# Kernel tuning notes

Measured on AMD Instinct MI355X. Metric: run time of the kernel, lower is better.

The kernel has to match this reference:

```python
import jax, jax.numpy as jnp
import numpy as np

DIM, HEADS, DHEAD = 256, 8, 64
INNER = HEADS * DHEAD
EPS = 1e-5


def _ln(x, g, b):
    m = x.mean(-1, keepdims=True)
    v = ((x - m) ** 2).mean(-1, keepdims=True)
    return (x - m) / jnp.sqrt(v + EPS) * g + b


def setup_inputs() -> dict:
    key = jax.random.key(0)
    ks = jax.random.split(key, 24)
    b, n, Q, K = 1, 6, 900, 1408
    d = DIM
    s = lambda fan_in: 1.0 / np.sqrt(fan_in)
    inp = {
        "k_g": jax.random.normal(ks[0], (b, n, K, d), jnp.float32),
        "q_g": jax.random.normal(ks[1], (b, n, Q, d), jnp.float32),
        "k_a": jax.random.normal(ks[2], (b, n, K, d), jnp.float32),
        "q_a": jax.random.normal(ks[3], (b, Q, d), jnp.float32),
        "v": jax.random.normal(ks[4], (b, n, K, d), jnp.float32),
        "mask": jax.random.randint(ks[5], (b, n, K), 0, 2).astype(bool),
        # projections (stored as (in, out))
        "W_qg": jax.random.uniform(ks[6], (d, INNER), jnp.float32, -s(d), s(d)),
        "b_qg": jnp.zeros((INNER,), jnp.float32),
        "W_kg": jax.random.uniform(ks[7], (d, INNER), jnp.float32, -s(d), s(d)),
        "b_kg": jnp.zeros((INNER,), jnp.float32),
        "W_qa": jax.random.uniform(ks[8], (d, INNER), jnp.float32, -s(d), s(d)),
        "b_qa": jnp.zeros((INNER,), jnp.float32),
        "W_ka": jax.random.uniform(ks[9], (d, INNER), jnp.float32, -s(d), s(d)),
        "b_ka": jnp.zeros((INNER,), jnp.float32),
        "W_v": jax.random.uniform(ks[10], (d, INNER), jnp.float32, -s(d), s(d)),
        "b_v": jnp.zeros((INNER,), jnp.float32),
        "W_o": jax.random.uniform(ks[11], (INNER, d), jnp.float32, -s(INNER), s(INNER)),
        "b_o": jnp.zeros((d,), jnp.float32),
        "ln1_g": jnp.ones((d,), jnp.float32),
        "ln1_b": jnp.zeros((d,), jnp.float32),
        "W_m1": jax.random.uniform(ks[12], (d, 2 * d), jnp.float32, -s(d), s(d)),
        "b_m1": jnp.zeros((2 * d,), jnp.float32),
        "W_m2": jax.random.uniform(ks[13], (2 * d, d), jnp.float32, -s(2 * d), s(2 * d)),
        "b_m2": jnp.zeros((d,), jnp.float32),
        "ln2_g": jnp.ones((d,), jnp.float32),
        "ln2_b": jnp.zeros((d,), jnp.float32),
        "scale_g": jnp.full((HEADS,), DHEAD ** -0.5, jnp.float32),
        "scale_a": jnp.full((HEADS,), DHEAD ** -0.5, jnp.float32),
    }
    return inp


def reference(k_g, q_g, k_a, q_a, v, mask,
              W_qg, b_qg, W_kg, b_kg, W_qa, b_qa, W_ka, b_ka, W_v, b_v,
              W_o, b_o, ln1_g, ln1_b, W_m1, b_m1, W_m2, b_m2, ln2_g, ln2_b,
              scale_g, scale_a):
    b, n, Q, _ = q_g.shape
    K = k_g.shape[2]
    h, dh = HEADS, DHEAD
    skip = q_a

    def split(x):  # (..., h*dh) -> (b, h, ..., dh)
        return jnp.moveaxis(x.reshape(x.shape[:-1] + (h, dh)), -2, 1)

    kg = split(k_g @ W_kg + b_kg)          # (b, h, n, K, dh)
    qg = split(q_g @ W_qg + b_qg)          # (b, h, n, Q, dh)
    ka = split(k_a @ W_ka + b_ka)          # (b, h, n, K, dh)
    qa = split(q_a @ W_qa + b_qa)          # (b, h, Q, dh)
    vv = split(v @ W_v + b_v)              # (b, h, n, K, dh)

    dot_g = jnp.einsum('bhnqd,bhnkd->bhnqk', qg, kg)
    dot_a = jnp.einsum('bhqd,bhnkd->bhnqk', qa, ka)
    sg = scale_g[None, :, None, None, None]
    sa = scale_a[None, :, None, None, None]
    dot = sg * dot_g + sa * dot_a
    dot = jnp.where(mask[:, None, :, None, :], -jnp.inf, dot)

    # softmax jointly over (n, K)
    dot = dot.transpose(0, 1, 3, 2, 4).reshape(b, h, Q, n * K)
    att = jax.nn.softmax(dot, axis=-1)
    vflat = vv.reshape(b, h, n * K, dh)
    a = jnp.einsum('bhqk,bhkd->bhqd', att, vflat)
    a = a.transpose(0, 2, 1, 3).reshape(b, Q, h * dh)

    z = a @ W_o + b_o + skip
    z = _ln(z, ln1_g, ln1_b)
    z = z + (jax.nn.gelu(z @ W_m1 + b_m1, approximate=False) @ W_m2 + b_m2)
    z = _ln(z, ln2_g, ln2_b)
    return z
```

## Files before the change

kernel.cpp:

```cpp
#include <hip/hip_runtime.h>
#include <stdint.h>

typedef unsigned short u16;
typedef _Float16 half8 __attribute__((ext_vector_type(8)));
typedef float f32x4 __attribute__((ext_vector_type(4)));

__device__ __forceinline__ u16 f2h(float f) {
    _Float16 h = (_Float16)f; u16 u; __builtin_memcpy(&u, &h, 2); return u;
}
__device__ __forceinline__ float h2f(u16 u) {
    _Float16 h; __builtin_memcpy(&h, &u, 2); return (float)h;
}

template<int CTRL>
__device__ __forceinline__ float dppf(float x) {
    return __builtin_bit_cast(float,
        __builtin_amdgcn_update_dpp(0, __builtin_bit_cast(int, x), CTRL, 0xF, 0xF, false));
}
__device__ __forceinline__ float sum16(float x) {
    x += dppf<0xB1>(x);
    x += dppf<0x4E>(x);
    x += dppf<0x124>(x);
    x += dppf<0x128>(x);
    return x;
}

__global__ __launch_bounds__(256) void prep_kernel(
    const float* __restrict__ W_qg, const float* __restrict__ W_kg,
    const float* __restrict__ W_qa, const float* __restrict__ W_ka,
    const float* __restrict__ W_v,  const float* __restrict__ W_o,
    const float* __restrict__ W_m1, const float* __restrict__ W_m2,
    u16* __restrict__ T_qg, u16* __restrict__ T_kg, u16* __restrict__ T_qa,
    u16* __restrict__ T_ka, u16* __restrict__ T_v,  u16* __restrict__ T_o,
    u16* __restrict__ T_m1, u16* __restrict__ T_m2,
    const float* __restrict__ scale_g, const float* __restrict__ scale_a,
    const float* __restrict__ b_kg, const float* __restrict__ b_ka,
    float* __restrict__ bkg_s, float* __restrict__ bka_s,
    const int* __restrict__ mask, int* __restrict__ mflag)
{
    const int z = blockIdx.z;
    const int tid = threadIdx.x;
    if (z == 8) {
        if (blockIdx.y != 0) return;
        if (blockIdx.x == 0) {
            __shared__ int f;
            if (tid == 0) f = 0;
            __syncthreads();
            int local = 0;
            for (int i = tid; i < 2112; i += 256) { int vv = mask[i]; if (vv & ~1) local = 1; }
            if (local) atomicOr(&f, 1);
            __syncthreads();
            if (tid == 0) *mflag = f;
        } else if (blockIdx.x == 1) {
            for (int j = tid; j < 512; j += 256) {
                bkg_s[j] = b_kg[j] * scale_g[j >> 6];
                bka_s[j] = b_ka[j] * scale_a[j >> 6];
            }
        }
        return;
    }
    const int K = (z == 5 || z == 7) ? 512 : 256;
    const int N = (z == 5 || z == 7) ? 256 : 512;
    const int k0 = blockIdx.x * 64, n0 = blockIdx.y * 64;
    if (k0 >= K || n0 >= N) return;
    const float* W = z==0?W_qg: z==1?W_kg: z==2?W_qa: z==3?W_ka: z==4?W_v: z==5?W_o: z==6?W_m1: W_m2;
    u16* D        = z==0?T_qg: z==1?T_kg: z==2?T_qa: z==3?T_ka: z==4?T_v: z==5?T_o: z==6?T_m1: T_m2;
    const float* scp = z==1 ? scale_g : z==3 ? scale_a : nullptr;

    __shared__ u16 T[64][80];
    const int cr = tid >> 4, cc = (tid & 15) * 4;
    const float sc = scp ? scp[(n0 + cc) >> 6] : 1.0f;
    #pragma unroll
    for (int i = 0; i < 4; ++i) {
        const int r = cr + i * 16;
        const float4 vv = *(const float4*)(W + (size_t)(k0 + r) * N + n0 + cc);
        T[cc + 0][r] = f2h(vv.x * sc);
        T[cc + 1][r] = f2h(vv.y * sc);
        T[cc + 2][r] = f2h(vv.z * sc);
        T[cc + 3][r] = f2h(vv.w * sc);
    }
    __syncthreads();
    const int nr = tid >> 2, part = (tid & 3) * 16;
    u16* drow = D + (size_t)(n0 + nr) * K + k0 + part;
    *(half8*)(drow)     = *(const half8*)&T[nr][part];
    *(half8*)(drow + 8) = *(const half8*)&T[nr][part + 8];
}

__global__ __launch_bounds__(256, 4) void proj_all(
    const float* __restrict__ k_g, const float* __restrict__ k_a,
    const float* __restrict__ v,   const float* __restrict__ q_g,
    const float* __restrict__ q_a,
    const u16* __restrict__ T_kg, const u16* __restrict__ T_ka,
    const u16* __restrict__ T_v,  const u16* __restrict__ T_qg,
    const u16* __restrict__ T_qa,
    const float* __restrict__ bkg_s, const float* __restrict__ bka_s,
    const float* __restrict__ b_v,   const float* __restrict__ b_qg,
    const float* __restrict__ b_qa,
    u16* __restrict__ qcat, u16* __restrict__ kcat, u16* __restrict__ vt)
{
    __shared__ u16 Ws[256 * 36];

    int bx = blockIdx.x;
    int mode, M;
    const float* X; const u16* Wt; const float* bias; u16* out;
    if (bx < 132)      { mode = 2; M = 8448; X = k_g; Wt = T_kg; bias = bkg_s; out = kcat; }
    else if (bx < 264) { mode = 3; M = 8448; X = k_a; Wt = T_ka; bias = bka_s; out = kcat; bx -= 132; }
    else if (bx < 396) { mode = 4; M = 8448; X = v;   Wt = T_v;  bias = b_v;   out = vt;   bx -= 264; }
    else if (bx < 481) { mode = 0; M = 5400; X = q_g; Wt = T_qg; bias = b_qg;  out = qcat; bx -= 396; }
    else               { mode = 1; M = 900;  X = q_a; Wt = T_qa; bias = b_qa;  out = qcat; bx -= 481; }
    const int rows_per_n = (mode == 0) ? 900 : 1408;

    const int tid = threadIdx.x;
    const int w = tid >> 6, lane = tid & 63;
    const int l15 = lane & 15, quad = lane >> 4;
    const int m0 = bx * 64;
    const int nbase = blockIdx.y * 256;
    const int row = m0 + w * 16 + l15;

    const float* xrow = X + (size_t)(row < M ? row : 0) * 256 + quad * 8;
    const u16* wcol = Wt + ((size_t)(nbase + tid) << 8);

    f32x4 o[4][4];
    #pragma unroll
    for (int nt = 0; nt < 4; ++nt)
        #pragma unroll
        for (int t = 0; t < 4; ++t) { o[nt][t][0]=0.f; o[nt][t][1]=0.f; o[nt][t][2]=0.f; o[nt][t][3]=0.f; }

    for (int k0 = 0; k0 < 8; ++k0) {
        {
            const uint4 w0 = *(const uint4*)(wcol + k0 * 32 + 0);
            const uint4 w1 = *(const uint4*)(wcol + k0 * 32 + 8);
            const uint4 w2 = *(const uint4*)(wcol + k0 * 32 + 16);
            const uint4 w3 = *(const uint4*)(wcol + k0 * 32 + 24);
            *(uint4*)&Ws[tid * 36 + 0]  = w0;
            *(uint4*)&Ws[tid * 36 + 8]  = w1;
            *(uint4*)&Ws[tid * 36 + 16] = w2;
            *(uint4*)&Ws[tid * 36 + 24] = w3;
        }
        __syncthreads();

        const float4 a0 = *(const float4*)(xrow + k0 * 32);
        const float4 a1 = *(const float4*)(xrow + k0 * 32 + 4);
        half8 af;
        af[0]=(_Float16)a0.x; af[1]=(_Float16)a0.y; af[2]=(_Float16)a0.z; af[3]=(_Float16)a0.w;
        af[4]=(_Float16)a1.x; af[5]=(_Float16)a1.y; af[6]=(_Float16)a1.z; af[7]=(_Float16)a1.w;

        #pragma unroll
        for (int nt = 0; nt < 4; ++nt)
            #pragma unroll
            for (int t = 0; t < 4; ++t) {
                const half8 bf = *(const half8*)&Ws[(nt * 64 + t * 16 + l15) * 36 + quad * 8];
                o[nt][t] = __builtin_amdgcn_mfma_f32_16x16x32_f16(af, bf, o[nt][t], 0, 0, 0);
            }
        __syncthreads();
    }

    #pragma unroll
    for (int nt = 0; nt < 4; ++nt) {
        const int n0 = nbase + nt * 64;
        const int hh = n0 >> 6;
        float bj[4];
        #pragma unroll
        for (int t = 0; t < 4; ++t) bj[t] = bias[n0 + t * 16 + l15];

        if (mode == 4) {
            const int gr0 = m0 + w * 16 + quad * 4;
            if (gr0 < M) {
                const int nI = gr0 / rows_per_n;
                const int rr = gr0 - nI * rows_per_n;
                u16* vb = out + (size_t)(hh * 6 + nI) * 64 * 1408;
                #pragma unroll
                for (int t = 0; t < 4; ++t) {
                    const int d = t * 16 + l15;
                    ushort4 pk;
                    pk.x = f2h(o[nt][t][0] + bj[t]);
                    pk.y = f2h(o[nt][t][1] + bj[t]);
                    pk.z = f2h(o[nt][t][2] + bj[t]);
                    pk.w = f2h(o[nt][t][3] + bj[t]);
                    *(ushort4*)&vb[(size_t)d * 1408 + rr] = pk;
                }
            }
        } else if (mode == 1) {
            #pragma unroll
            for (int r = 0; r < 4; ++r) {
                const int gr = m0 + w * 16 + quad * 4 + r;
                if (gr < M) {
                    for (int nb = 0; nb < 6; ++nb) {
                        u16* qb = out + (((size_t)(hh * 6 + nb) * 900 + gr) << 7) + 64;
                        #pragma unroll
                        for (int t = 0; t < 4; ++t)
                            qb[t * 16 + l15] = f2h(o[nt][t][r] + bj[t]);
                    }
                }
            }
        } else {
            const size_t kdim = (mode == 0) ? 900 : 1408;
            const int doff = (mode == 3) ? 64 : 0;
            #pragma unroll
            for (int r = 0; r < 4; ++r) {
                const int gr = m0 + w * 16 + quad * 4 + r;
                if (gr < M) {
                    const int nI = gr / rows_per_n;
                    const int rr = gr - nI * rows_per_n;
                    u16* ob = out + (((size_t)(hh * 6 + nI) * kdim + rr) << 7) + doff;
                    #pragma unroll
                    for (int t = 0; t < 4; ++t)
                        ob[t * 16 + l15] = f2h(o[nt][t][r] + bj[t]);
                }
            }
        }
    }
}

__global__ __launch_bounds__(256, 4) void attn_kernel(
    const u16* __restrict__ qcat, const u16* __restrict__ kcat,
    const u16* __restrict__ vt, const void* __restrict__ maskp,
    const int* __restrict__ mflag,
    u16* __restrict__ Opart, float* __restrict__ lpart)
{
    __shared__ __align__(16) u16 Ks[64 * 136];
    __shared__ __align__(16) u16 Vs[64 * 72];
    __shared__ __align__(16) u16 Ps[4][1216];
    __shared__ float Mb[64];

    const int flat = blockIdx.x;
    const int grp = flat >> 3;
    const int qt = grp % 15;
    const int rest = grp / 15;
    const int hn_i = (flat & 7) + 8 * (rest % 6);
    const int sp = rest / 6;
    const int h = hn_i / 6, n = hn_i - h * 6;
    (void)h;

    const int q0 = qt * 64;
    const int tid = threadIdx.x;
    const int w = tid >> 6, lane = tid & 63;
    const int l15 = lane & 15, quad = lane >> 4;
    const bool m8 = (*mflag != 0);
    const size_t hn = (size_t)hn_i;

    const u16* kbase = kcat + ((hn * 1408) << 7);
    const u16* vbase = vt + hn * 64 * 1408;
    const unsigned char* mB = (const unsigned char*)maskp;
    const int* mI = (const int*)maskp;
    const int mko = n * 1408;

    const int krow_s = tid >> 4;
    const int kcol_s = (tid & 15) * 8;
    const int vrow_s = tid >> 3;
    const int vcol_s = (tid & 7) * 8;

    half8 qf[4];
    {
        const int gq = q0 + w * 16 + l15;
        if (gq < 900) {
            const u16* qrow = qcat + ((hn * 900 + gq) << 7) + quad * 8;
            #pragma unroll
            for (int k0 = 0; k0 < 4; ++k0)
                qf[k0] = *(const half8*)(qrow + k0 * 32);
        } else {
            #pragma unroll
            for (int k0 = 0; k0 < 4; ++k0)
                #pragma unroll
                for (int j = 0; j < 8; ++j) qf[k0][j] = (_Float16)0.0f;
        }
    }

    half8 onesb;
    {
        const _Float16 ov = (l15 == 0) ? (_Float16)1.0f : (_Float16)0.0f;
        #pragma unroll
        for (int j = 0; j < 8; ++j) onesb[j] = ov;
    }

    f32x4 o[4];
    f32x4 l16;
    #pragma unroll
    for (int t = 0; t < 4; ++t) { o[t][0]=0.f; o[t][1]=0.f; o[t][2]=0.f; o[t][3]=0.f; }
    l16[0]=0.f; l16[1]=0.f; l16[2]=0.f; l16[3]=0.f;

    uint4 kA, kB, kC, kD, vA, vB;
    float mreg = 0.0f;
    {
        const int k0c = (sp * 11) * 64;
        kA = *(const uint4*)(kbase + ((size_t)(k0c +  0 + krow_s) << 7) + kcol_s);
        kB = *(const uint4*)(kbase + ((size_t)(k0c + 16 + krow_s) << 7) + kcol_s);
        kC = *(const uint4*)(kbase + ((size_t)(k0c + 32 + krow_s) << 7) + kcol_s);
        kD = *(const uint4*)(kbase + ((size_t)(k0c + 48 + krow_s) << 7) + kcol_s);
        vA = *(const uint4*)(vbase + (size_t)(vrow_s)      * 1408 + k0c + vcol_s);
        vB = *(const uint4*)(vbase + (size_t)(32 + vrow_s) * 1408 + k0c + vcol_s);
        if (tid < 64) {
            const int ki = mko + k0c + tid;
            const int mv = m8 ? (int)mB[ki] : mI[ki];
            mreg = mv ? -1e30f : 0.0f;
        }
    }

    for (int cc = 0; cc < 11; ++cc) {
        *(uint4*)&Ks[( 0 + krow_s) * 136 + kcol_s] = kA;
        *(uint4*)&Ks[(16 + krow_s) * 136 + kcol_s] = kB;
        *(uint4*)&Ks[(32 + krow_s) * 136 + kcol_s] = kC;
        *(uint4*)&Ks[(48 + krow_s) * 136 + kcol_s] = kD;
        *(uint4*)&Vs[(vrow_s)      * 72 + vcol_s] = vA;
        *(uint4*)&Vs[(32 + vrow_s) * 72 + vcol_s] = vB;
        if (tid < 64) Mb[tid] = mreg;
        __syncthreads();

        if (cc < 10) {
            const int k0n = (sp * 11 + cc + 1) * 64;
            kA = *(const uint4*)(kbase + ((size_t)(k0n +  0 + krow_s) << 7) + kcol_s);
            kB = *(const uint4*)(kbase + ((size_t)(k0n + 16 + krow_s) << 7) + kcol_s);
            kC = *(const uint4*)(kbase + ((size_t)(k0n + 32 + krow_s) << 7) + kcol_s);
            kD = *(const uint4*)(kbase + ((size_t)(k0n + 48 + krow_s) << 7) + kcol_s);
            vA = *(const uint4*)(vbase + (size_t)(vrow_s)      * 1408 + k0n + vcol_s);
            vB = *(const uint4*)(vbase + (size_t)(32 + vrow_s) * 1408 + k0n + vcol_s);
            if (tid < 64) {
                const int ki = mko + k0n + tid;
                const int mv = m8 ? (int)mB[ki] : mI[ki];
                mreg = mv ? -1e30f : 0.0f;
            }
        }

        f32x4 s[4];
        #pragma unroll
        for (int t = 0; t < 4; ++t) {
            const float mbv = Mb[t * 16 + l15];
            s[t][0]=mbv; s[t][1]=mbv; s[t][2]=mbv; s[t][3]=mbv;
        }
        #pragma unroll
        for (int k0 = 0; k0 < 4; ++k0)
            #pragma unroll
            for (int t = 0; t < 4; ++t) {
                const half8 kf = *(const half8*)&Ks[(t * 16 + l15) * 136 + k0 * 32 + quad * 8];
                s[t] = __builtin_amdgcn_mfma_f32_16x16x32_f16(qf[k0], kf, s[t], 0, 0, 0);
            }

        #pragma unroll
        for (int r = 0; r < 4; ++r) {
            const float p0 = __expf(s[0][r]);
            const float p1 = __expf(s[1][r]);
            const float p2 = __expf(s[2][r]);
            const float p3 = __expf(s[3][r]);
            u16* pr = &Ps[w][(quad * 4 + r) * 72 + quad * 16 + l15];
            pr[0]  = f2h(p0);
            pr[16] = f2h(p1);
            pr[32] = f2h(p2);
            pr[48] = f2h(p3);
        }

        const u16* prow = &Ps[w][l15 * 72 + (l15 >> 2) * 16 + quad * 8];
        const half8 pa0 = *(const half8*)(prow);
        const half8 pa1 = *(const half8*)(prow + 32);

        l16 = __builtin_amdgcn_mfma_f32_16x16x32_f16(pa0, onesb, l16, 0, 0, 0);
        l16 = __builtin_amdgcn_mfma_f32_16x16x32_f16(pa1, onesb, l16, 0, 0, 0);

        #pragma unroll
        for (int t = 0; t < 4; ++t) {
            const half8 v0 = *(const half8*)&Vs[(t * 16 + l15) * 72 + quad * 8];
            const half8 v1 = *(const half8*)&Vs[(t * 16 + l15) * 72 + 32 + quad * 8];
            o[t] = __builtin_amdgcn_mfma_f32_16x16x32_f16(pa0, v0, o[t], 0, 0, 0);
            o[t] = __builtin_amdgcn_mfma_f32_16x16x32_f16(pa1, v1, o[t], 0, 0, 0);
        }
        __syncthreads();
    }

    const int p = sp * 48 + hn_i;
    #pragma unroll
    for (int r = 0; r < 4; ++r) {
        const int gq = q0 + w * 16 + quad * 4 + r;
        if (gq < 900) {
            u16* db = Opart + ((size_t)p * 900 + gq) * 64 + l15;
            db[0]  = f2h(o[0][r]);
            db[16] = f2h(o[1][r]);
            db[32] = f2h(o[2][r]);
            db[48] = f2h(o[3][r]);
            if (l15 == 0) lpart[p * 900 + gq] = l16[r];
        }
    }
}

__global__ __launch_bounds__(256) void combine_kernel(
    const u16* __restrict__ Opart, const float* __restrict__ lpart,
    u16* __restrict__ a16)
{
    const int g = blockIdx.x * 256 + threadIdx.x;
    const int h = g / 57600;
    const int r = g - h * 57600;
    const int q = r >> 6;
    const int d = r & 63;
    float l = 0.f, ov = 0.f;
    #pragma unroll
    for (int s = 0; s < 12; ++s) {
        const int p = (s >> 1) + h * 6 + ((s & 1) ? 48 : 0);
        l  += lpart[p * 900 + q];
        ov += h2f(Opart[((size_t)p * 900 + q) * 64 + d]);
    }
    a16[(size_t)q * 512 + h * 64 + d] = f2h(ov / fmaxf(l, 1e-30f));
}

__global__ __launch_bounds__(256) void epi_mega(
    const u16* __restrict__ a16, const u16* __restrict__ T_o,
    const u16* __restrict__ T_m1, const u16* __restrict__ T_m2,
    const float* __restrict__ b_o, const float* __restrict__ q_a,
    const float* __restrict__ ln1_g, const float* __restrict__ ln1_b,
    const float* __restrict__ b_m1, const float* __restrict__ b_m2,
    const float* __restrict__ ln2_g, const float* __restrict__ ln2_b,
    float* __restrict__ outf)
{
    __shared__ u16 Z1[16][264];
    __shared__ u16 H[16][520];
    __shared__ float Ssum[4][16];
    __shared__ float Ssq[4][16];

    const int tid = threadIdx.x;
    const int w = tid >> 6, lane = tid & 63;
    const int l15 = lane & 15, quad = lane >> 4;
    const int m0 = blockIdx.x * 16;

    {
        const int ar = m0 + l15;
        const u16* arow = a16 + (size_t)(ar < 900 ? ar : 899) * 512 + quad * 8;

        f32x4 acc[4];
        #pragma unroll
        for (int t = 0; t < 4; ++t) { acc[t][0]=0.f; acc[t][1]=0.f; acc[t][2]=0.f; acc[t][3]=0.f; }

        #pragma unroll
        for (int k0 = 0; k0 < 16; ++k0) {
            const half8 af = *(const half8*)(arow + k0 * 32);
            #pragma unroll
            for (int t = 0; t < 4; ++t) {
                const int nn = w * 64 + t * 16 + l15;
                const half8 bf = *(const half8*)(T_o + (size_t)nn * 512 + k0 * 32 + quad * 8);
                acc[t] = __builtin_amdgcn_mfma_f32_16x16x32_f16(af, bf, acc[t], 0, 0, 0);
            }
        }

        float vals[4][4];
        #pragma unroll
        for (int r = 0; r < 4; ++r) {
            const int row = m0 + quad * 4 + r;
            const int rows = row < 900 ? row : 899;
            float s = 0.f, sq = 0.f;
            #pragma unroll
            for (int t = 0; t < 4; ++t) {
                const int col = w * 64 + t * 16 + l15;
                const float x = acc[t][r] + b_o[col] + q_a[(size_t)rows * 256 + col];
                vals[r][t] = x; s += x; sq += x * x;
            }
            s = sum16(s); sq = sum16(sq);
            if (l15 == 0) { Ssum[w][quad * 4 + r] = s; Ssq[w][quad * 4 + r] = sq; }
        }
        __syncthreads();

        #pragma unroll
        for (int r = 0; r < 4; ++r) {
            const int rl = quad * 4 + r;
            const float st = Ssum[0][rl] + Ssum[1][rl] + Ssum[2][rl] + Ssum[3][rl];
            const float qt = Ssq[0][rl] + Ssq[1][rl] + Ssq[2][rl] + Ssq[3][rl];
            const float mean = st * (1.0f / 256.0f);
            const float var  = qt * (1.0f / 256.0f) - mean * mean;
            const float inv  = rsqrtf(var + 1e-5f);
            #pragma unroll
            for (int t = 0; t < 4; ++t) {
                const int col = w * 64 + t * 16 + l15;
                const float z = (vals[r][t] - mean) * inv * ln1_g[col] + ln1_b[col];
                Z1[rl][col] = f2h(z);
            }
        }
        __syncthreads();
    }

    {
        f32x4 acc[8];
        #pragma unroll
        for (int t = 0; t < 8; ++t) { acc[t][0]=0.f; acc[t][1]=0.f; acc[t][2]=0.f; acc[t][3]=0.f; }

        #pragma unroll
        for (int k0 = 0; k0 < 8; ++k0) {
            const half8 af = *(const half8*)&Z1[l15][k0 * 32 + quad * 8];
            #pragma unroll
            for (int t = 0; t < 8; ++t) {
                const int nn = w * 128 + t * 16 + l15;
                const half8 bf = *(const half8*)(T_m1 + (size_t)nn * 256 + k0 * 32 + quad * 8);
                acc[t] = __builtin_amdgcn_mfma_f32_16x16x32_f16(af, bf, acc[t], 0, 0, 0);
            }
        }

        #pragma unroll
        for (int r = 0; r < 4; ++r) {
            const int rl = quad * 4 + r;
            #pragma unroll
            for (int t = 0; t < 8; ++t) {
                const int col = w * 128 + t * 16 + l15;
                const float x = acc[t][r] + b_m1[col];
                H[rl][col] = f2h(0.5f * x * (1.0f + erff(x * 0.70710678118654752f)));
            }
        }
        __syncthreads();
    }

    {
        f32x4 acc[4];
        #pragma unroll
        for (int t = 0; t < 4; ++t) { acc[t][0]=0.f; acc[t][1]=0.f; acc[t][2]=0.f; acc[t][3]=0.f; }

        #pragma unroll
        for (int k0 = 0; k0 < 16; ++k0) {
            const half8 af = *(const half8*)&H[l15][k0 * 32 + quad * 8];
            #pragma unroll
            for (int t = 0; t < 4; ++t) {
                const int nn = w * 64 + t * 16 + l15;
                const half8 bf = *(const half8*)(T_m2 + (size_t)nn * 512 + k0 * 32 + quad * 8);
                acc[t] = __builtin_amdgcn_mfma_f32_16x16x32_f16(af, bf, acc[t], 0, 0, 0);
            }
        }

        float vals[4][4];
        #pragma unroll
        for (int r = 0; r < 4; ++r) {
            const int rl = quad * 4 + r;
            float s = 0.f, sq = 0.f;
            #pragma unroll
            for (int t = 0; t < 4; ++t) {
                const int col = w * 64 + t * 16 + l15;
                const float x = acc[t][r] + b_m2[col] + h2f(Z1[rl][col]);
                vals[r][t] = x; s += x; sq += x * x;
            }
            s = sum16(s); sq = sum16(sq);
            if (l15 == 0) { Ssum[w][rl] = s; Ssq[w][rl] = sq; }
        }
        __syncthreads();

        #pragma unroll
        for (int r = 0; r < 4; ++r) {
            const int rl = quad * 4 + r;
            const float st = Ssum[0][rl] + Ssum[1][rl] + Ssum[2][rl] + Ssum[3][rl];
            const float qt = Ssq[0][rl] + Ssq[1][rl] + Ssq[2][rl] + Ssq[3][rl];
            const float mean = st * (1.0f / 256.0f);
            const float var  = qt * (1.0f / 256.0f) - mean * mean;
            const float inv  = rsqrtf(var + 1e-5f);
            const int row = m0 + rl;
            if (row < 900) {
                #pragma unroll
                for (int t = 0; t < 4; ++t) {
                    const int col = w * 64 + t * 16 + l15;
                    outf[(size_t)row * 256 + col] = (vals[r][t] - mean) * inv * ln2_g[col] + ln2_b[col];
                }
            }
        }
    }
}

extern "C" void kernel_launch(void* const* d_in, const int* in_sizes, int n_in,
                              void* d_out, int out_size, void* d_ws, size_t ws_size,
                              hipStream_t stream)
{
    const float* k_g  = (const float*)d_in[0];
    const float* q_g  = (const float*)d_in[1];
    const float* k_a  = (const float*)d_in[2];
    const float* q_a  = (const float*)d_in[3];
    const float* v    = (const float*)d_in[4];
    const void*  mask = d_in[5];
    const float* W_qg = (const float*)d_in[6];
    const float* b_qg = (const float*)d_in[7];
    const float* W_kg = (const float*)d_in[8];
    const float* b_kg = (const float*)d_in[9];
    const float* W_qa = (const float*)d_in[10];
    const float* b_qa = (const float*)d_in[11];
    const float* W_ka = (const float*)d_in[12];
    const float* b_ka = (const float*)d_in[13];
    const float* W_v  = (const float*)d_in[14];
    const float* b_v  = (const float*)d_in[15];
    const float* W_o  = (const float*)d_in[16];
    const float* b_o  = (const float*)d_in[17];
    const float* ln1_g = (const float*)d_in[18];
    const float* ln1_b = (const float*)d_in[19];
    const float* W_m1 = (const float*)d_in[20];
    const float* b_m1 = (const float*)d_in[21];
    const float* W_m2 = (const float*)d_in[22];
    const float* b_m2 = (const float*)d_in[23];
    const float* ln2_g = (const float*)d_in[24];
    const float* ln2_b = (const float*)d_in[25];
    const float* scale_g = (const float*)d_in[26];
    const float* scale_a = (const float*)d_in[27];

    char* ws = (char*)d_ws;
    size_t off = 0;
    auto alloc = [&](size_t bytes) -> void* {
        void* p = ws + off;
        off += (bytes + 255) & ~(size_t)255;
        return p;
    };
    u16*   qcat  = (u16*)  alloc((size_t)8 * 6 * 900  * 128 * 2);
    u16*   kcat  = (u16*)  alloc((size_t)8 * 6 * 1408 * 128 * 2);
    u16*   vt    = (u16*)  alloc((size_t)8 * 6 * 64 * 1408 * 2);
    u16*   a16   = (u16*)  alloc((size_t)900 * 512 * 2);
    u16*   Tw[8];
    for (int i = 0; i < 8; ++i) Tw[i] = (u16*)alloc((size_t)512 * 256 * 2);
    float* bkg_s = (float*)alloc((size_t)512 * 4);
    float* bka_s = (float*)alloc((size_t)512 * 4);
    int*   mflag = (int*)  alloc(256);
    u16*   Opart = (u16*)  alloc((size_t)96 * 900 * 64 * 2);
    float* lpart = (float*)alloc((size_t)96 * 900 * 4);

    prep_kernel<<<dim3(8, 8, 9), 256, 0, stream>>>(
        W_qg, W_kg, W_qa, W_ka, W_v, W_o, W_m1, W_m2,
        Tw[0], Tw[1], Tw[2], Tw[3], Tw[4], Tw[5], Tw[6], Tw[7],
        scale_g, scale_a, b_kg, b_ka, bkg_s, bka_s, (const int*)mask, mflag);

    proj_all<<<dim3(496, 2), 256, 0, stream>>>(
        k_g, k_a, v, q_g, q_a,
        Tw[1], Tw[3], Tw[4], Tw[0], Tw[2],
        bkg_s, bka_s, b_v, b_qg, b_qa,
        qcat, kcat, vt);

    attn_kernel<<<1440, 256, 0, stream>>>(qcat, kcat, vt, mask, mflag, Opart, lpart);
    combine_kernel<<<1800, 256, 0, stream>>>(Opart, lpart, a16);

    epi_mega<<<57, 256, 0, stream>>>(
        a16, Tw[5], Tw[6], Tw[7],
        b_o, q_a, ln1_g, ln1_b, b_m1, b_m2, ln2_g, ln2_b,
        (float*)d_out);
}
```

Baseline: 244.7 us.

## Restructure attention to split keys across waves and drop K-split partials

Attention blocks now cover all 22 key chunks, and the two-way split over the key dimension is removed. Each wave owns 16 keys of a chunk and computes all 64 queries, with the transposed S = K·Q^T feeding P directly from registers into 16x16x16 MFMAs. This removes the shared-memory P round trip and the ones-vector MFMA for the row sums. Partial outputs from the four waves are reduced through shared memory at the end, and the combine kernel is vectorized over half the partials. The epilogue launches more blocks with 4 rows each, trading lower attention grid parallelism and more registers for less LDS traffic and fewer partials.

```diff
diff --git a/kernel.cpp b/kernel.cpp
--- a/kernel.cpp
+++ b/kernel.cpp
@@ -3,6 +3,8 @@
 
 typedef unsigned short u16;
 typedef _Float16 half8 __attribute__((ext_vector_type(8)));
+typedef _Float16 half4 __attribute__((ext_vector_type(4)));
+typedef _Float16 half2 __attribute__((ext_vector_type(2)));
 typedef float f32x4 __attribute__((ext_vector_type(4)));
 
 __device__ __forceinline__ u16 f2h(float f) {
@@ -212,25 +214,21 @@
     }
 }
 
-__global__ __launch_bounds__(256, 4) void attn_kernel(
+__global__ __launch_bounds__(256, 2) void attn_kernel(
     const u16* __restrict__ qcat, const u16* __restrict__ kcat,
     const u16* __restrict__ vt, const void* __restrict__ maskp,
     const int* __restrict__ mflag,
     u16* __restrict__ Opart, float* __restrict__ lpart)
 {
-    __shared__ __align__(16) u16 Ks[64 * 136];
-    __shared__ __align__(16) u16 Vs[64 * 72];
-    __shared__ __align__(16) u16 Ps[4][1216];
+    __shared__ __align__(16) u16 SMEM[64 * 136 + 64 * 72];
     __shared__ float Mb[64];
+    u16* Ks = SMEM;
+    u16* Vs = SMEM + 64 * 136;
 
     const int flat = blockIdx.x;
-    const int grp = flat >> 3;
-    const int qt = grp % 15;
-    const int rest = grp / 15;
-    const int hn_i = (flat & 7) + 8 * (rest % 6);
-    const int sp = rest / 6;
-    const int h = hn_i / 6, n = hn_i - h * 6;
-    (void)h;
+    const int hn_i = (flat & 7) + 8 * ((flat >> 3) % 6);
+    const int qt = flat / 48;
+    const int n = hn_i - (hn_i / 6) * 6;
 
     const int q0 = qt * 64;
     const int tid = threadIdx.x;
@@ -250,53 +248,49 @@
     const int vrow_s = tid >> 3;
     const int vcol_s = (tid & 7) * 8;
 
-    half8 qf[4];
-    {
-        const int gq = q0 + w * 16 + l15;
+    half8 qf[4][4];
+    #pragma unroll
+    for (int qq = 0; qq < 4; ++qq) {
+        const int gq = q0 + qq * 16 + l15;
         if (gq < 900) {
             const u16* qrow = qcat + ((hn * 900 + gq) << 7) + quad * 8;
             #pragma unroll
             for (int k0 = 0; k0 < 4; ++k0)
-                qf[k0] = *(const half8*)(qrow + k0 * 32);
+                qf[qq][k0] = *(const half8*)(qrow + k0 * 32);
         } else {
             #pragma unroll
             for (int k0 = 0; k0 < 4; ++k0)
                 #pragma unroll
-                for (int j = 0; j < 8; ++j) qf[k0][j] = (_Float16)0.0f;
-        }
-    }
-
-    half8 onesb;
-    {
-        const _Float16 ov = (l15 == 0) ? (_Float16)1.0f : (_Float16)0.0f;
-        #pragma unroll
-        for (int j = 0; j < 8; ++j) onesb[j] = ov;
-    }
-
-    f32x4 o[4];
-    f32x4 l16;
-    #pragma unroll
-    for (int t = 0; t < 4; ++t) { o[t][0]=0.f; o[t][1]=0.f; o[t][2]=0.f; o[t][3]=0.f; }
-    l16[0]=0.f; l16[1]=0.f; l16[2]=0.f; l16[3]=0.f;
+                for (int j = 0; j < 8; ++j) qf[qq][k0][j] = (_Float16)0.0f;
+        }
+    }
+
+    f32x4 o[4][4];
+    float lacc[4];
+    #pragma unroll
+    for (int dt = 0; dt < 4; ++dt)
+        #pragma unroll
+        for (int qq = 0; qq < 4; ++qq) { o[dt][qq][0]=0.f; o[dt][qq][1]=0.f; o[dt][qq][2]=0.f; o[dt][qq][3]=0.f; }
+    #pragma unroll
+    for (int qq = 0; qq < 4; ++qq) lacc[qq] = 0.f;
 
     uint4 kA, kB, kC, kD, vA, vB;
     float mreg = 0.0f;
     {
-        const int k0c = (sp * 11) * 64;
-        kA = *(const uint4*)(kbase + ((size_t)(k0c +  0 + krow_s) << 7) + kcol_s);
-        kB = *(const uint4*)(kbase + ((size_t)(k0c + 16 + krow_s) << 7) + kcol_s);
-        kC = *(const uint4*)(kbase + ((size_t)(k0c + 32 + krow_s) << 7) + kcol_s);
-        kD = *(const uint4*)(kbase + ((size_t)(k0c + 48 + krow_s) << 7) + kcol_s);
-        vA = *(const uint4*)(vbase + (size_t)(vrow_s)      * 1408 + k0c + vcol_s);
-        vB = *(const uint4*)(vbase + (size_t)(32 + vrow_s) * 1408 + k0c + vcol_s);
+        kA = *(const uint4*)(kbase + ((size_t)( 0 + krow_s) << 7) + kcol_s);
+        kB = *(const uint4*)(kbase + ((size_t)(16 + krow_s) << 7) + kcol_s);
+        kC = *(const uint4*)(kbase + ((size_t)(32 + krow_s) << 7) + kcol_s);
+        kD = *(const uint4*)(kbase + ((size_t)(48 + krow_s) << 7) + kcol_s);
+        vA = *(const uint4*)(vbase + (size_t)(vrow_s)      * 1408 + vcol_s);
+        vB = *(const uint4*)(vbase + (size_t)(32 + vrow_s) * 1408 + vcol_s);
         if (tid < 64) {
-            const int ki = mko + k0c + tid;
+            const int ki = mko + tid;
             const int mv = m8 ? (int)mB[ki] : mI[ki];
             mreg = mv ? -1e30f : 0.0f;
         }
     }
 
-    for (int cc = 0; cc < 11; ++cc) {
+    for (int cc = 0; cc < 22; ++cc) {
         *(uint4*)&Ks[( 0 + krow_s) * 136 + kcol_s] = kA;
         *(uint4*)&Ks[(16 + krow_s) * 136 + kcol_s] = kB;
         *(uint4*)&Ks[(32 + krow_s) * 136 + kcol_s] = kC;
@@ -306,8 +300,8 @@
         if (tid < 64) Mb[tid] = mreg;
         __syncthreads();
 
-        if (cc < 10) {
-            const int k0n = (sp * 11 + cc + 1) * 64;
+        if (cc < 21) {
+            const int k0n = (cc + 1) * 64;
             kA = *(const uint4*)(kbase + ((size_t)(k0n +  0 + krow_s) << 7) + kcol_s);
             kB = *(const uint4*)(kbase + ((size_t)(k0n + 16 + krow_s) << 7) + kcol_s);
             kC = *(const uint4*)(kbase + ((size_t)(k0n + 32 + krow_s) << 7) + kcol_s);
@@ -321,61 +315,87 @@
             }
         }
 
+        float mb[4];
+        #pragma unroll
+        for (int r = 0; r < 4; ++r) mb[r] = Mb[w * 16 + quad * 4 + r];
+
         f32x4 s[4];
         #pragma unroll
-        for (int t = 0; t < 4; ++t) {
-            const float mbv = Mb[t * 16 + l15];
-            s[t][0]=mbv; s[t][1]=mbv; s[t][2]=mbv; s[t][3]=mbv;
-        }
-        #pragma unroll
-        for (int k0 = 0; k0 < 4; ++k0)
-            #pragma unroll
-            for (int t = 0; t < 4; ++t) {
-                const half8 kf = *(const half8*)&Ks[(t * 16 + l15) * 136 + k0 * 32 + quad * 8];
-                s[t] = __builtin_amdgcn_mfma_f32_16x16x32_f16(qf[k0], kf, s[t], 0, 0, 0);
-            }
-
-        #pragma unroll
-        for (int r = 0; r < 4; ++r) {
-            const float p0 = __expf(s[0][r]);
-            const float p1 = __expf(s[1][r]);
-            const float p2 = __expf(s[2][r]);
-            const float p3 = __expf(s[3][r]);
-            u16* pr = &Ps[w][(quad * 4 + r) * 72 + quad * 16 + l15];
-            pr[0]  = f2h(p0);
-            pr[16] = f2h(p1);
-            pr[32] = f2h(p2);
-            pr[48] = f2h(p3);
-        }
-
-        const u16* prow = &Ps[w][l15 * 72 + (l15 >> 2) * 16 + quad * 8];
-        const half8 pa0 = *(const half8*)(prow);
-        const half8 pa1 = *(const half8*)(prow + 32);
-
-        l16 = __builtin_amdgcn_mfma_f32_16x16x32_f16(pa0, onesb, l16, 0, 0, 0);
-        l16 = __builtin_amdgcn_mfma_f32_16x16x32_f16(pa1, onesb, l16, 0, 0, 0);
-
-        #pragma unroll
-        for (int t = 0; t < 4; ++t) {
-            const half8 v0 = *(const half8*)&Vs[(t * 16 + l15) * 72 + quad * 8];
-            const half8 v1 = *(const half8*)&Vs[(t * 16 + l15) * 72 + 32 + quad * 8];
-            o[t] = __builtin_amdgcn_mfma_f32_16x16x32_f16(pa0, v0, o[t], 0, 0, 0);
-            o[t] = __builtin_amdgcn_mfma_f32_16x16x32_f16(pa1, v1, o[t], 0, 0, 0);
-        }
-        __syncthreads();
-    }
-
-    const int p = sp * 48 + hn_i;
-    #pragma unroll
-    for (int r = 0; r < 4; ++r) {
-        const int gq = q0 + w * 16 + quad * 4 + r;
-        if (gq < 900) {
-            u16* db = Opart + ((size_t)p * 900 + gq) * 64 + l15;
-            db[0]  = f2h(o[0][r]);
-            db[16] = f2h(o[1][r]);
-            db[32] = f2h(o[2][r]);
-            db[48] = f2h(o[3][r]);
-            if (l15 == 0) lpart[p * 900 + gq] = l16[r];
+        for (int qq = 0; qq < 4; ++qq) { s[qq][0]=mb[0]; s[qq][1]=mb[1]; s[qq][2]=mb[2]; s[qq][3]=mb[3]; }
+
+        #pragma unroll
+        for (int k0 = 0; k0 < 4; ++k0) {
+            const half8 kf = *(const half8*)&Ks[(w * 16 + l15) * 136 + k0 * 32 + quad * 8];
+            #pragma unroll
+            for (int qq = 0; qq < 4; ++qq)
+                s[qq] = __builtin_amdgcn_mfma_f32_16x16x32_f16(kf, qf[qq][k0], s[qq], 0, 0, 0);
+        }
+
+        half4 pf[4];
+        #pragma unroll
+        for (int qq = 0; qq < 4; ++qq) {
+            const float p0 = __expf(s[qq][0]);
+            const float p1 = __expf(s[qq][1]);
+            const float p2 = __expf(s[qq][2]);
+            const float p3 = __expf(s[qq][3]);
+            lacc[qq] += (p0 + p1) + (p2 + p3);
+            const half2 lo = __builtin_bit_cast(half2, __builtin_amdgcn_cvt_pkrtz(p0, p1));
+            const half2 hi = __builtin_bit_cast(half2, __builtin_amdgcn_cvt_pkrtz(p2, p3));
+            half4 pk; pk[0]=lo[0]; pk[1]=lo[1]; pk[2]=hi[0]; pk[3]=hi[1];
+            pf[qq] = pk;
+        }
+
+        #pragma unroll
+        for (int dt = 0; dt < 4; ++dt) {
+            const half4 vf = *(const half4*)&Vs[(dt * 16 + l15) * 72 + w * 16 + quad * 4];
+            #pragma unroll
+            for (int qq = 0; qq < 4; ++qq)
+                o[dt][qq] = __builtin_amdgcn_mfma_f32_16x16x16f16(vf, pf[qq], o[dt][qq], 0, 0, 0);
+        }
+        __syncthreads();
+    }
+
+    __syncthreads();
+    float* Red = (float*)SMEM;
+    float* Lp  = (float*)(SMEM + 64 * 136);
+
+    #pragma unroll
+    for (int qq = 0; qq < 4; ++qq)
+        Lp[(w * 4 + quad) * 64 + qq * 16 + l15] = lacc[qq];
+    #pragma unroll
+    for (int qq = 0; qq < 4; ++qq)
+        #pragma unroll
+        for (int r = 0; r < 4; ++r)
+            Red[(w * 16 + quad * 4 + r) * 68 + qq * 16 + l15] = o[0][qq][r];
+    __syncthreads();
+
+    if (tid < 64) {
+        float l = 0.f;
+        #pragma unroll
+        for (int i = 0; i < 16; ++i) l += Lp[i * 64 + tid];
+        if (q0 + tid < 900) lpart[hn_i * 900 + q0 + tid] = l;
+    }
+
+    const int dloc = tid & 15, qgrp = tid >> 4;
+    #pragma unroll
+    for (int dt = 0; dt < 4; ++dt) {
+        #pragma unroll
+        for (int i = 0; i < 4; ++i) {
+            const int q = qgrp * 4 + i;
+            const float sum = Red[( 0 + dloc) * 68 + q] + Red[(16 + dloc) * 68 + q]
+                            + Red[(32 + dloc) * 68 + q] + Red[(48 + dloc) * 68 + q];
+            const int gq = q0 + q;
+            if (gq < 900)
+                Opart[((size_t)hn_i * 900 + gq) * 64 + dt * 16 + dloc] = f2h(sum);
+        }
+        if (dt < 3) {
+            __syncthreads();
+            #pragma unroll
+            for (int qq = 0; qq < 4; ++qq)
+                #pragma unroll
+                for (int r = 0; r < 4; ++r)
+                    Red[(w * 16 + quad * 4 + r) * 68 + qq * 16 + l15] = o[dt + 1][qq][r];
+            __syncthreads();
         }
     }
 }
@@ -385,18 +405,24 @@
     u16* __restrict__ a16)
 {
     const int g = blockIdx.x * 256 + threadIdx.x;
-    const int h = g / 57600;
-    const int r = g - h * 57600;
-    const int q = r >> 6;
-    const int d = r & 63;
-    float l = 0.f, ov = 0.f;
-    #pragma unroll
-    for (int s = 0; s < 12; ++s) {
-        const int p = (s >> 1) + h * 6 + ((s & 1) ? 48 : 0);
-        l  += lpart[p * 900 + q];
-        ov += h2f(Opart[((size_t)p * 900 + q) * 64 + d]);
-    }
-    a16[(size_t)q * 512 + h * 64 + d] = f2h(ov / fmaxf(l, 1e-30f));
+    const int h = g / 14400;
+    const int r = g - h * 14400;
+    const int q = r >> 4;
+    const int d4 = (r & 15) * 4;
+    float l = 0.f;
+    float o0 = 0.f, o1 = 0.f, o2 = 0.f, o3 = 0.f;
+    #pragma unroll
+    for (int s = 0; s < 6; ++s) {
+        const int p = h * 6 + s;
+        l += lpart[p * 900 + q];
+        const ushort4 t = *(const ushort4*)&Opart[((size_t)p * 900 + q) * 64 + d4];
+        o0 += h2f(t.x); o1 += h2f(t.y); o2 += h2f(t.z); o3 += h2f(t.w);
+    }
+    const float inv = 1.0f / fmaxf(l, 1e-30f);
+    ushort4 outp;
+    outp.x = f2h(o0 * inv); outp.y = f2h(o1 * inv);
+    outp.z = f2h(o2 * inv); outp.w = f2h(o3 * inv);
+    *(ushort4*)&a16[(size_t)q * 512 + h * 64 + d4] = outp;
 }
 
 __global__ __launch_bounds__(256) void epi_mega(
@@ -416,7 +442,7 @@
     const int tid = threadIdx.x;
     const int w = tid >> 6, lane = tid & 63;
     const int l15 = lane & 15, quad = lane >> 4;
-    const int m0 = blockIdx.x * 16;
+    const int m0 = blockIdx.x * 4;
 
     {
         const int ar = m0 + l15;
@@ -542,7 +568,7 @@
             const float var  = qt * (1.0f / 256.0f) - mean * mean;
             const float inv  = rsqrtf(var + 1e-5f);
             const int row = m0 + rl;
-            if (row < 900) {
+            if (rl < 4 && row < 900) {
                 #pragma unroll
                 for (int t = 0; t < 4; ++t) {
                     const int col = w * 64 + t * 16 + l15;
@@ -602,8 +628,8 @@
     float* bkg_s = (float*)alloc((size_t)512 * 4);
     float* bka_s = (float*)alloc((size_t)512 * 4);
     int*   mflag = (int*)  alloc(256);
-    u16*   Opart = (u16*)  alloc((size_t)96 * 900 * 64 * 2);
-    float* lpart = (float*)alloc((size_t)96 * 900 * 4);
+    u16*   Opart = (u16*)  alloc((size_t)48 * 900 * 64 * 2);
+    float* lpart = (float*)alloc((size_t)48 * 900 * 4);
 
     prep_kernel<<<dim3(8, 8, 9), 256, 0, stream>>>(
         W_qg, W_kg, W_qa, W_ka, W_v, W_o, W_m1, W_m2,
@@ -616,10 +642,10 @@
         bkg_s, bka_s, b_v, b_qg, b_qa,
         qcat, kcat, vt);
 
-    attn_kernel<<<1440, 256, 0, stream>>>(qcat, kcat, vt, mask, mflag, Opart, lpart);
-    combine_kernel<<<1800, 256, 0, stream>>>(Opart, lpart, a16);
-
-    epi_mega<<<57, 256, 0, stream>>>(
+    attn_kernel<<<720, 256, 0, stream>>>(qcat, kcat, vt, mask, mflag, Opart, lpart);
+    combine_kernel<<<450, 256, 0, stream>>>(Opart, lpart, a16);
+
+    epi_mega<<<225, 256, 0, stream>>>(
         a16, Tw[5], Tw[6], Tw[7],
         b_o, q_a, ln1_g, ln1_b, b_m1, b_m2, ln2_g, ln2_b,
         (float*)d_out);
```

New measurement: 256.9 us. +5.0%, slower.

## Fuse split-K combine into epilogue kernel with 4-row tiles

Applied to the files above, without the earlier changes.

Removes the separate combine kernel and performs the partial-output reduction (sum of 12 partials, divide by l) inside the epilogue, staging the normalized attention rows in shared memory. The epilogue tile shrinks from 16 rows to 4 rows so 225 blocks cover the 900 queries instead of 57, and each block's 16-row MFMA operand repeats the 4 real rows. This saves a kernel launch and the a16 round-trip through global memory and raises block count. The cost is that three quarters of the MFMA work is redundant, and the weight matrices are re-read by four times as many blocks.

```diff
diff --git a/kernel.cpp b/kernel.cpp
--- a/kernel.cpp
+++ b/kernel.cpp
@@ -3,6 +3,8 @@
 
 typedef unsigned short u16;
 typedef _Float16 half8 __attribute__((ext_vector_type(8)));
+typedef _Float16 half4 __attribute__((ext_vector_type(4)));
+typedef _Float16 half2 __attribute__((ext_vector_type(2)));
 typedef float f32x4 __attribute__((ext_vector_type(4)));
 
 __device__ __forceinline__ u16 f2h(float f) {
@@ -282,7 +284,7 @@
     uint4 kA, kB, kC, kD, vA, vB;
     float mreg = 0.0f;
     {
-        const int k0c = (sp * 11) * 64;
+        const int k0c = sp * 11 * 64;
         kA = *(const uint4*)(kbase + ((size_t)(k0c +  0 + krow_s) << 7) + kcol_s);
         kB = *(const uint4*)(kbase + ((size_t)(k0c + 16 + krow_s) << 7) + kcol_s);
         kC = *(const uint4*)(kbase + ((size_t)(k0c + 32 + krow_s) << 7) + kcol_s);
@@ -380,27 +382,9 @@
     }
 }
 
-__global__ __launch_bounds__(256) void combine_kernel(
+__global__ __launch_bounds__(256) void epi_mega(
     const u16* __restrict__ Opart, const float* __restrict__ lpart,
-    u16* __restrict__ a16)
-{
-    const int g = blockIdx.x * 256 + threadIdx.x;
-    const int h = g / 57600;
-    const int r = g - h * 57600;
-    const int q = r >> 6;
-    const int d = r & 63;
-    float l = 0.f, ov = 0.f;
-    #pragma unroll
-    for (int s = 0; s < 12; ++s) {
-        const int p = (s >> 1) + h * 6 + ((s & 1) ? 48 : 0);
-        l  += lpart[p * 900 + q];
-        ov += h2f(Opart[((size_t)p * 900 + q) * 64 + d]);
-    }
-    a16[(size_t)q * 512 + h * 64 + d] = f2h(ov / fmaxf(l, 1e-30f));
-}
-
-__global__ __launch_bounds__(256) void epi_mega(
-    const u16* __restrict__ a16, const u16* __restrict__ T_o,
+    const u16* __restrict__ T_o,
     const u16* __restrict__ T_m1, const u16* __restrict__ T_m2,
     const float* __restrict__ b_o, const float* __restrict__ q_a,
     const float* __restrict__ ln1_g, const float* __restrict__ ln1_b,
@@ -408,6 +392,7 @@
     const float* __restrict__ ln2_g, const float* __restrict__ ln2_b,
     float* __restrict__ outf)
 {
+    __shared__ u16 A16[4][520];
     __shared__ u16 Z1[16][264];
     __shared__ u16 H[16][520];
     __shared__ float Ssum[4][16];
@@ -416,19 +401,44 @@
     const int tid = threadIdx.x;
     const int w = tid >> 6, lane = tid & 63;
     const int l15 = lane & 15, quad = lane >> 4;
-    const int m0 = blockIdx.x * 16;
+    const int m0 = blockIdx.x * 4;
 
     {
-        const int ar = m0 + l15;
-        const u16* arow = a16 + (size_t)(ar < 900 ? ar : 899) * 512 + quad * 8;
-
+        const int r = tid >> 6;
+        const int cg = tid & 63;
+        const int c8 = cg * 8;
+        const int hh = cg >> 3;
+        const int d8 = c8 & 56;
+        const int q = m0 + r;
+        float l = 0.f;
+        float a0=0.f,a1=0.f,a2=0.f,a3=0.f,a4=0.f,a5=0.f,a6=0.f,a7=0.f;
+        #pragma unroll
+        for (int s = 0; s < 12; ++s) {
+            const int p = ((s & 1) ? 48 : 0) + hh * 6 + (s >> 1);
+            l += lpart[p * 900 + q];
+            const u16* ob = Opart + ((size_t)p * 900 + q) * 64 + d8;
+            const ushort4 t0 = *(const ushort4*)ob;
+            const ushort4 t1 = *(const ushort4*)(ob + 4);
+            a0 += h2f(t0.x); a1 += h2f(t0.y); a2 += h2f(t0.z); a3 += h2f(t0.w);
+            a4 += h2f(t1.x); a5 += h2f(t1.y); a6 += h2f(t1.z); a7 += h2f(t1.w);
+        }
+        const float inv = 1.0f / fmaxf(l, 1e-30f);
+        ushort4 o0, o1;
+        o0.x = f2h(a0 * inv); o0.y = f2h(a1 * inv); o0.z = f2h(a2 * inv); o0.w = f2h(a3 * inv);
+        o1.x = f2h(a4 * inv); o1.y = f2h(a5 * inv); o1.z = f2h(a6 * inv); o1.w = f2h(a7 * inv);
+        *(ushort4*)&A16[r][c8]     = o0;
+        *(ushort4*)&A16[r][c8 + 4] = o1;
+    }
+    __syncthreads();
+
+    {
         f32x4 acc[4];
         #pragma unroll
         for (int t = 0; t < 4; ++t) { acc[t][0]=0.f; acc[t][1]=0.f; acc[t][2]=0.f; acc[t][3]=0.f; }
 
         #pragma unroll
         for (int k0 = 0; k0 < 16; ++k0) {
-            const half8 af = *(const half8*)(arow + k0 * 32);
+            const half8 af = *(const half8*)&A16[l15 & 3][k0 * 32 + quad * 8];
             #pragma unroll
             for (int t = 0; t < 4; ++t) {
                 const int nn = w * 64 + t * 16 + l15;
@@ -440,13 +450,12 @@
         float vals[4][4];
         #pragma unroll
         for (int r = 0; r < 4; ++r) {
-            const int row = m0 + quad * 4 + r;
-            const int rows = row < 900 ? row : 899;
+            const int row = m0 + ((quad * 4 + r) & 3);
             float s = 0.f, sq = 0.f;
             #pragma unroll
             for (int t = 0; t < 4; ++t) {
                 const int col = w * 64 + t * 16 + l15;
-                const float x = acc[t][r] + b_o[col] + q_a[(size_t)rows * 256 + col];
+                const float x = acc[t][r] + b_o[col] + q_a[(size_t)row * 256 + col];
                 vals[r][t] = x; s += x; sq += x * x;
             }
             s = sum16(s); sq = sum16(sq);
@@ -542,7 +551,7 @@
             const float var  = qt * (1.0f / 256.0f) - mean * mean;
             const float inv  = rsqrtf(var + 1e-5f);
             const int row = m0 + rl;
-            if (row < 900) {
+            if (rl < 4 && row < 900) {
                 #pragma unroll
                 for (int t = 0; t < 4; ++t) {
                     const int col = w * 64 + t * 16 + l15;
@@ -596,7 +605,6 @@
     u16*   qcat  = (u16*)  alloc((size_t)8 * 6 * 900  * 128 * 2);
     u16*   kcat  = (u16*)  alloc((size_t)8 * 6 * 1408 * 128 * 2);
     u16*   vt    = (u16*)  alloc((size_t)8 * 6 * 64 * 1408 * 2);
-    u16*   a16   = (u16*)  alloc((size_t)900 * 512 * 2);
     u16*   Tw[8];
     for (int i = 0; i < 8; ++i) Tw[i] = (u16*)alloc((size_t)512 * 256 * 2);
     float* bkg_s = (float*)alloc((size_t)512 * 4);
@@ -617,10 +625,9 @@
         qcat, kcat, vt);
 
     attn_kernel<<<1440, 256, 0, stream>>>(qcat, kcat, vt, mask, mflag, Opart, lpart);
-    combine_kernel<<<1800, 256, 0, stream>>>(Opart, lpart, a16);
-
-    epi_mega<<<57, 256, 0, stream>>>(
-        a16, Tw[5], Tw[6], Tw[7],
+
+    epi_mega<<<225, 256, 0, stream>>>(
+        Opart, lpart, Tw[5], Tw[6], Tw[7],
         b_o, q_a, ln1_g, ln1_b, b_m1, b_m2, ln2_g, ln2_b,
         (float*)d_out);
 }
```

After: 241.7 us. About the same (-1.3%).
